# Performance work log

Hardware: AMD Instinct MI355X
Metric: run time of the kernel (lower is better)

The kernel has to match this reference:

```python
import jax, jax.numpy as jnp
import numpy as np

D_MODEL = 1024
N_HEADS = 16
D_K = D_MODEL // N_HEADS


def setup_inputs() -> dict:
    key = jax.random.key(0)
    k1, k2, k3 = jax.random.split(key, 3)
    x = jax.random.normal(k1, (4, 2048, D_MODEL), dtype=jnp.float32)
    # torch nn.Linear(d, 3d, bias=False): y = x @ W.T ; we store W.T directly as (in, out)
    w_qkv = jax.random.normal(k2, (D_MODEL, 3 * D_MODEL), dtype=jnp.float32) * (1.0 / np.sqrt(D_MODEL))
    w_out = jax.random.normal(k3, (D_MODEL, D_MODEL), dtype=jnp.float32) * (1.0 / np.sqrt(D_MODEL))
    return {"x": x, "w_qkv": w_qkv, "w_out": w_out}


def reference(x, w_qkv, w_out):
    B, T, D = x.shape
    qkv = jnp.einsum('btd,de->bte', x, w_qkv)  # (B,T,3D)
    q, k, v = jnp.split(qkv, 3, axis=-1)
    # split heads -> (B,H,T,d_k)
    def split_heads(t):
        return t.reshape(B, T, N_HEADS, D_K).transpose(0, 2, 1, 3)
    q, k, v = split_heads(q), split_heads(k), split_heads(v)
    scale = 1.0 / np.sqrt(D_K).astype(np.float32)
    scores = jnp.einsum('bhqd,bhkd->bhqk', q, k) * scale  # (B,H,T,T)
    causal = jnp.triu(jnp.full((T, T), -jnp.inf, dtype=scores.dtype), k=1)
    scores = scores + causal[None, None]
    weights = jax.nn.softmax(scores, axis=-1)
    attn = jnp.einsum('bhqk,bhkd->bhqd', weights, v)
    attn = attn.transpose(0, 2, 1, 3).reshape(B, T, D)
    return jnp.einsum('btd,de->bte', attn, w_out)
```

## Files before the change

kernel.cpp:

```cpp
#include <hip/hip_runtime.h>
#include <hip/hip_bf16.h>

typedef short short8 __attribute__((ext_vector_type(8)));
typedef float f32x4 __attribute__((ext_vector_type(4)));
typedef float f32x16 __attribute__((ext_vector_type(16)));

#define MFMA16(a, b, c) __builtin_amdgcn_mfma_f32_16x16x32_bf16((a), (b), (c), 0, 0, 0)
#define MFMA32(a, b, c) __builtin_amdgcn_mfma_f32_32x32x16_bf16((a), (b), (c), 0, 0, 0)

#define GLOAD16(gp, lp)                                                    \
    __builtin_amdgcn_global_load_lds(                                      \
        (const __attribute__((address_space(1))) unsigned int*)(gp),       \
        (__attribute__((address_space(3))) unsigned int*)(lp), 16, 0, 0)

__device__ __forceinline__ unsigned short f2b(float x) {
    unsigned int u = __float_as_uint(x);
    unsigned int r = u + 0x7FFFu + ((u >> 16) & 1u);
    return (unsigned short)(r >> 16);
}

#if __has_builtin(__builtin_amdgcn_cvt_pk_bf16_f32)
__device__ __forceinline__ unsigned pack2(float a, float b) {
    auto v = __builtin_amdgcn_cvt_pk_bf16_f32(a, b);
    unsigned u;
    __builtin_memcpy(&u, &v, 4);
    return u;
}
#else
__device__ __forceinline__ unsigned pack2(float a, float b) {
    return (unsigned)f2b(a) | ((unsigned)f2b(b) << 16);
}
#endif

__global__ __launch_bounds__(256) void cast4_kernel(const float* __restrict__ in,
                                                    unsigned short* __restrict__ out,
                                                    int n4) {
    int i = blockIdx.x * 256 + threadIdx.x;
    if (i < n4) {
        float4 v = ((const float4*)in)[i];
        ushort4 o;
        o.x = f2b(v.x); o.y = f2b(v.y); o.z = f2b(v.z); o.w = f2b(v.w);
        ((ushort4*)out)[i] = o;
    }
}

__global__ __launch_bounds__(256) void transpose_cast_f32(const float* __restrict__ in,
                                                          unsigned short* __restrict__ out,
                                                          int K, int N) {
    __shared__ unsigned short Ls[64 * 66];
    const int k0 = blockIdx.y * 64, n0 = blockIdx.x * 64;
    const int tid = threadIdx.x;
    const int krow = tid >> 4, nc4 = (tid & 15) * 4;
#pragma unroll
    for (int p = 0; p < 4; p++) {
        float4 v = *(const float4*)(in + (size_t)(k0 + krow + p * 16) * N + n0 + nc4);
        unsigned* d32 = (unsigned*)(Ls + (krow + p * 16) * 66 + nc4);
        d32[0] = pack2(v.x, v.y);
        d32[1] = pack2(v.z, v.w);
    }
    __syncthreads();
    const int n = tid >> 3, kc = (tid & 7) * 8;
#pragma unroll
    for (int p = 0; p < 2; p++) {
        int nn = n + p * 32;
        unsigned short w[8];
#pragma unroll
        for (int j = 0; j < 8; j++) w[j] = Ls[(kc + j) * 66 + nn];
        *(short8*)(out + (size_t)(n0 + nn) * K + k0 + kc) = *(short8*)w;
    }
}

__global__ __launch_bounds__(256) void gemm_qkv(const unsigned short* __restrict__ A,
                                                const unsigned short* __restrict__ Bt,
                                                unsigned short* __restrict__ Qb,
                                                unsigned short* __restrict__ Kb,
                                                unsigned short* __restrict__ Vt) {
    const int K = 1024, lda = 1024;
    __shared__ unsigned short As[128 * 64];
    __shared__ unsigned short Bs[128 * 64];

    const int tid  = threadIdx.x;
    const int wave = tid >> 6;
    const int lane = tid & 63;
    const int l32  = lane & 31;
    const int hi   = lane >> 5;
    const int m0 = blockIdx.y * 128;
    const int n0 = blockIdx.x * 128;
    const int wm = (wave >> 1) * 64;
    const int wn = (wave & 1) * 64;

    const int rl = lane >> 3;
    const int sc = ((lane & 7) ^ rl) * 8;

    const unsigned short* Ag[4]; unsigned short* Al[4];
    const unsigned short* Bg[4]; unsigned short* Bl[4];
#pragma unroll
    for (int cc = 0; cc < 4; cc++) {
        Ag[cc] = A  + (size_t)(m0 + wave * 32 + cc * 8 + rl) * lda + sc;
        Bg[cc] = Bt + (size_t)(n0 + wave * 32 + cc * 8 + rl) * K + sc;
        Al[cc] = As + (wave * 4 + cc) * 512;
        Bl[cc] = Bs + (wave * 4 + cc) * 512;
    }

    f32x16 acc[2][2] = {};

    for (int k0 = 0; k0 < K; k0 += 64) {
        __syncthreads();
#pragma unroll
        for (int cc = 0; cc < 4; cc++) GLOAD16(Ag[cc] + k0, Al[cc]);
#pragma unroll
        for (int cc = 0; cc < 4; cc++) GLOAD16(Bg[cc] + k0, Bl[cc]);
        __syncthreads();

#pragma unroll
        for (int ks = 0; ks < 4; ks++) {
            const int ch = (((ks * 2 + hi) ^ (l32 & 7))) * 8;
            short8 a0 = *(const short8*)(As + (wm + l32) * 64 + ch);
            short8 a1 = *(const short8*)(As + (wm + 32 + l32) * 64 + ch);
            short8 b0 = *(const short8*)(Bs + (wn + l32) * 64 + ch);
            short8 b1 = *(const short8*)(Bs + (wn + 32 + l32) * 64 + ch);
            acc[0][0] = MFMA32(a0, b0, acc[0][0]);
            acc[0][1] = MFMA32(a0, b1, acc[0][1]);
            acc[1][0] = MFMA32(a1, b0, acc[1][0]);
            acc[1][1] = MFMA32(a1, b1, acc[1][1]);
        }
    }

    if (n0 < 2048) {
        unsigned short* outp = (n0 < 1024) ? Qb : Kb;
        const int cb = (n0 < 1024) ? n0 : n0 - 1024;
        const float QS = (n0 < 1024) ? 0.125f * 1.44269504f : 1.0f;
#pragma unroll
        for (int i = 0; i < 2; i++)
#pragma unroll
            for (int j = 0; j < 2; j++)
#pragma unroll
                for (int r = 0; r < 16; r++) {
                    int row = m0 + wm + i * 32 + (r & 3) + 8 * (r >> 2) + 4 * hi;
                    int col = cb + wn + j * 32 + l32;
                    outp[(size_t)row * 1024 + col] = f2b(acc[i][j][r] * QS);
                }
    } else {
        const int b = m0 >> 11;
        const int t0b = m0 & 2047;
        const int hbase = (n0 - 2048) >> 6;
        unsigned short* smem = As;
        __syncthreads();
#pragma unroll
        for (int p = 0; p < 2; p++) {
            if ((wave & 1) == p) {
#pragma unroll
                for (int i = 0; i < 2; i++)
#pragma unroll
                    for (int j = 0; j < 2; j++) {
                        const int c = j * 32 + l32;
#pragma unroll
                        for (int rg = 0; rg < 4; rg++) {
                            const int rowbase = wm + i * 32 + rg * 8 + 4 * hi;
                            uint2 v;
                            v.x = pack2(acc[i][j][4 * rg + 0], acc[i][j][4 * rg + 1]);
                            v.y = pack2(acc[i][j][4 * rg + 2], acc[i][j][4 * rg + 3]);
                            const int w = c * 64 + ((rowbase >> 1) ^ (4 * (c & 7)));
                            *(uint2*)(smem + 2 * w) = v;
                        }
                    }
            }
            __syncthreads();
#pragma unroll
            for (int it = 0; it < 4; it++) {
                const int id = it * 256 + tid;
                const int c = id >> 4, rg = id & 15;
                const int w = c * 64 + ((rg * 4) ^ (4 * (c & 7)));
                short8 v = *(const short8*)(smem + 2 * w);
                const int h = hbase + p;
                *(short8*)(Vt + ((size_t)((b * 16 + h) * 64 + c)) * 2048 + t0b + rg * 8) = v;
            }
            __syncthreads();
        }
    }
}

__global__ __launch_bounds__(256) void gemm_out(const unsigned short* __restrict__ A,
                                                const unsigned short* __restrict__ Bt,
                                                float* __restrict__ C) {
    const int K = 1024, lda = 1024;
    __shared__ unsigned short As[64 * 64];
    __shared__ unsigned short Bs[128 * 64];

    const int tid  = threadIdx.x;
    const int wave = tid >> 6;
    const int lane = tid & 63;
    const int l32  = lane & 31;
    const int hi   = lane >> 5;
    const int m0 = blockIdx.y * 64;
    const int n0 = blockIdx.x * 128;
    const int wm = (wave >> 1) * 32;
    const int wn = (wave & 1) * 64;

    const int rl = lane >> 3;
    const int sc = ((lane & 7) ^ rl) * 8;

    const unsigned short* Ag[2]; unsigned short* Al[2];
#pragma unroll
    for (int cc = 0; cc < 2; cc++) {
        Ag[cc] = A + (size_t)(m0 + wave * 16 + cc * 8 + rl) * lda + sc;
        Al[cc] = As + (wave * 2 + cc) * 512;
    }
    const unsigned short* Bg[4]; unsigned short* Bl[4];
#pragma unroll
    for (int cc = 0; cc < 4; cc++) {
        Bg[cc] = Bt + (size_t)(n0 + wave * 32 + cc * 8 + rl) * K + sc;
        Bl[cc] = Bs + (wave * 4 + cc) * 512;
    }

    f32x16 acc[2] = {};

    for (int k0 = 0; k0 < K; k0 += 64) {
        __syncthreads();
#pragma unroll
        for (int cc = 0; cc < 2; cc++) GLOAD16(Ag[cc] + k0, Al[cc]);
#pragma unroll
        for (int cc = 0; cc < 4; cc++) GLOAD16(Bg[cc] + k0, Bl[cc]);
        __syncthreads();

#pragma unroll
        for (int ks = 0; ks < 4; ks++) {
            const int ch = (((ks * 2 + hi) ^ (l32 & 7))) * 8;
            short8 a  = *(const short8*)(As + (wm + l32) * 64 + ch);
            short8 b0 = *(const short8*)(Bs + (wn + l32) * 64 + ch);
            short8 b1 = *(const short8*)(Bs + (wn + 32 + l32) * 64 + ch);
            acc[0] = MFMA32(a, b0, acc[0]);
            acc[1] = MFMA32(a, b1, acc[1]);
        }
    }

#pragma unroll
    for (int j = 0; j < 2; j++)
#pragma unroll
        for (int r = 0; r < 16; r++) {
            int row = m0 + wm + (r & 3) + 8 * (r >> 2) + 4 * hi;
            int col = n0 + wn + j * 32 + l32;
            C[(size_t)row * 1024 + col] = acc[j][r];
        }
}

__global__ __launch_bounds__(256) void attention_kernel(const unsigned short* Qb,
                                                        const unsigned short* Kb,
                                                        const unsigned short* Vt,
                                                        unsigned short* attn) {
    const int T = 2048;
    const int bi = blockIdx.x;
    const int qb = 31 - (bi >> 6);
    const int hb = bi & 63;
    const int b = hb >> 4, h = hb & 15;
    const int qb0 = qb * 64;
    const int tid = threadIdx.x, wave = tid >> 6, lane = tid & 63;
    const int l16 = lane & 15, quad = lane >> 4;
    const int qw0 = qb0 + wave * 16;

    const unsigned short* Qp  = Qb + (size_t)b * T * 1024 + h * 64;
    const unsigned short* Kp  = Kb + (size_t)b * T * 1024 + h * 64;
    const unsigned short* Vbh = Vt + ((size_t)(b * 16 + h) * 64) * 2048;

    __shared__ unsigned short Ks[2][64 * 32];
    __shared__ unsigned short Vts[2][64 * 32];
    __shared__ unsigned short Ps[4][16 * 40];
    unsigned short* Psw = Ps[wave];

    short8 qf[2];
#pragma unroll
    for (int kd = 0; kd < 2; kd++)
        qf[kd] = *(const short8*)(Qp + (size_t)(qw0 + l16) * 1024 + kd * 32 + quad * 8);

    f32x4 o[4] = {};
    float l_acc = 0.f;

    const int srow = lane >> 2;
    const int scol = (((lane & 3) ^ ((lane >> 3) & 3)) * 8);
    const int sw8  = ((l16 >> 1) & 3) * 8;
    const size_t ktstep = (wave < 2) ? (size_t)64 * 1024 : (size_t)64;
    const size_t cstep  = (wave < 2) ? (size_t)16 * 1024 : (size_t)16 * T;
    const unsigned short* g0 = (wave < 2)
            ? Kp + (size_t)srow * 1024 + wave * 32 + scol
            : Vbh + (size_t)srow * T + (wave - 2) * 32 + scol;
    unsigned short* l0 = (wave < 2) ? Ks[wave] : Vts[wave - 2];

    for (int kt = 0; kt <= qb; kt++) {
        const int tk0 = kt * 64;
        const unsigned short* g = g0 + (size_t)kt * ktstep;
        __syncthreads();
#pragma unroll
        for (int c = 0; c < 4; c++) GLOAD16(g + c * cstep, l0 + c * 512);
        __syncthreads();

#pragma unroll
        for (int th = 0; th < 2; th++) {
            if (tk0 + th * 32 > qw0 + 15) continue;

            f32x4 s[2];
            bool act[2];
#pragma unroll
            for (int mi = 0; mi < 2; mi++) {
                const int t0 = tk0 + (th * 2 + mi) * 16;
                act[mi] = (t0 <= qw0 + 15);
                s[mi] = (f32x4){0.f, 0.f, 0.f, 0.f};
                if (act[mi]) {
                    const int row = (th * 2 + mi) * 16 + l16;
                    short8 kf0 = *(const short8*)(Ks[0] + row * 32 + (quad * 8 ^ sw8));
                    short8 kf1 = *(const short8*)(Ks[1] + row * 32 + (quad * 8 ^ sw8));
                    s[mi] = MFMA16(kf0, qf[0], s[mi]);
                    s[mi] = MFMA16(kf1, qf[1], s[mi]);
                }
            }
#pragma unroll
            for (int mi = 0; mi < 2; mi++) {
                const int t0 = tk0 + (th * 2 + mi) * 16;
                unsigned pk0 = 0, pk1 = 0;
                if (act[mi]) {
                    const bool full = (t0 + 15) <= qw0;
                    float p[4];
#pragma unroll
                    for (int r = 0; r < 4; r++) {
                        float e = __builtin_amdgcn_exp2f(s[mi][r]);
                        if (!full)
                            e = (t0 + quad * 4 + r <= qw0 + l16) ? e : 0.f;
                        p[r] = e;
                    }
                    l_acc += (p[0] + p[1]) + (p[2] + p[3]);
                    pk0 = pack2(p[0], p[1]);
                    pk1 = pack2(p[2], p[3]);
                }
                uint2 pr; pr.x = pk0; pr.y = pk1;
                *(uint2*)(Psw + l16 * 40 + mi * 16 + quad * 4) = pr;
            }
            short8 pf = *(const short8*)(Psw + l16 * 40 + quad * 8);
#pragma unroll
            for (int dt = 0; dt < 4; dt++) {
                short8 vf = *(const short8*)(Vts[th] + (dt * 16 + l16) * 32 + (quad * 8 ^ sw8));
                o[dt] = MFMA16(vf, pf, o[dt]);
            }
        }
    }

    float l = l_acc;
    l += __shfl_xor(l, 16);
    l += __shfl_xor(l, 32);
    const float rl2 = 1.f / l;
    const int q = qw0 + l16;
#pragma unroll
    for (int dt = 0; dt < 4; dt++) {
        ushort4 wv;
        wv.x = f2b(o[dt][0] * rl2);
        wv.y = f2b(o[dt][1] * rl2);
        wv.z = f2b(o[dt][2] * rl2);
        wv.w = f2b(o[dt][3] * rl2);
        *(ushort4*)(attn + (size_t)(b * T + q) * 1024 + h * 64 + dt * 16 + quad * 4) = wv;
    }
}

extern "C" void kernel_launch(void* const* d_in, const int* in_sizes, int n_in,
                              void* d_out, int out_size, void* d_ws, size_t ws_size,
                              hipStream_t stream) {
    const float* x     = (const float*)d_in[0];
    const float* w_qkv = (const float*)d_in[1];
    const float* w_out = (const float*)d_in[2];
    float* out = (float*)d_out;

    const int M = 8192, D = 1024, E = 3072;
    const size_t MB = 1048576;

    char* ws = (char*)d_ws;
    unsigned short* xb    = (unsigned short*)ws;
    unsigned short* wqkvT = (unsigned short*)(ws + 16 * MB);
    unsigned short* woutT = (unsigned short*)(ws + 22 * MB);
    unsigned short* Qb    = (unsigned short*)(ws + 24 * MB);
    unsigned short* Kb    = (unsigned short*)(ws + 40 * MB);
    unsigned short* Vt    = (unsigned short*)(ws + 56 * MB);

    cast4_kernel<<<M * D / 4 / 256, 256, 0, stream>>>(x, xb, M * D / 4);
    transpose_cast_f32<<<dim3(E / 64, D / 64), 256, 0, stream>>>(w_qkv, wqkvT, D, E);
    transpose_cast_f32<<<dim3(D / 64, D / 64), 256, 0, stream>>>(w_out, woutT, D, D);

    gemm_qkv<<<dim3(E / 128, M / 128), 256, 0, stream>>>(xb, wqkvT, Qb, Kb, Vt);

    attention_kernel<<<dim3(2048), 256, 0, stream>>>(Qb, Kb, Vt, Qb);

    gemm_out<<<dim3(D / 128, M / 64), 256, 0, stream>>>(Qb, woutT, out);
}
```

Measured before the change: 269.5 us.

## Double-buffer LDS tiles in GEMM and attention kernels to overlap loads

Converts the QKV GEMM, the output GEMM and the attention K/V loop from load-then-compute with two barriers per step to a double-buffered scheme. The next tile's global_load_lds is issued into the alternate buffer right after a single barrier, while the current buffer is consumed by MFMAs. This is meant to hide global-memory latency and remove one barrier per iteration. In exchange, shared memory per block roughly doubles, which may lower the number of resident blocks per CU.

```diff
diff --git a/kernel.cpp b/kernel.cpp
--- a/kernel.cpp
+++ b/kernel.cpp
@@ -76,8 +76,8 @@
                                                 unsigned short* __restrict__ Kb,
                                                 unsigned short* __restrict__ Vt) {
     const int K = 1024, lda = 1024;
-    __shared__ unsigned short As[128 * 64];
-    __shared__ unsigned short Bs[128 * 64];
+    __shared__ unsigned short As[2 * 8192];
+    __shared__ unsigned short Bs[2 * 8192];
 
     const int tid  = threadIdx.x;
     const int wave = tid >> 6;
@@ -104,21 +104,29 @@
 
     f32x16 acc[2][2] = {};
 
-    for (int k0 = 0; k0 < K; k0 += 64) {
+#pragma unroll
+    for (int cc = 0; cc < 4; cc++) GLOAD16(Ag[cc], Al[cc]);
+#pragma unroll
+    for (int cc = 0; cc < 4; cc++) GLOAD16(Bg[cc], Bl[cc]);
+
+    int buf = 0;
+    for (int k0 = 0; k0 < K; k0 += 64, buf ^= 1) {
         __syncthreads();
-#pragma unroll
-        for (int cc = 0; cc < 4; cc++) GLOAD16(Ag[cc] + k0, Al[cc]);
-#pragma unroll
-        for (int cc = 0; cc < 4; cc++) GLOAD16(Bg[cc] + k0, Bl[cc]);
-        __syncthreads();
-
+        if (k0 + 64 < K) {
+#pragma unroll
+            for (int cc = 0; cc < 4; cc++) GLOAD16(Ag[cc] + k0 + 64, Al[cc] + (buf ^ 1) * 8192);
+#pragma unroll
+            for (int cc = 0; cc < 4; cc++) GLOAD16(Bg[cc] + k0 + 64, Bl[cc] + (buf ^ 1) * 8192);
+        }
+        const unsigned short* Asb = As + buf * 8192;
+        const unsigned short* Bsb = Bs + buf * 8192;
 #pragma unroll
         for (int ks = 0; ks < 4; ks++) {
             const int ch = (((ks * 2 + hi) ^ (l32 & 7))) * 8;
-            short8 a0 = *(const short8*)(As + (wm + l32) * 64 + ch);
-            short8 a1 = *(const short8*)(As + (wm + 32 + l32) * 64 + ch);
-            short8 b0 = *(const short8*)(Bs + (wn + l32) * 64 + ch);
-            short8 b1 = *(const short8*)(Bs + (wn + 32 + l32) * 64 + ch);
+            short8 a0 = *(const short8*)(Asb + (wm + l32) * 64 + ch);
+            short8 a1 = *(const short8*)(Asb + (wm + 32 + l32) * 64 + ch);
+            short8 b0 = *(const short8*)(Bsb + (wn + l32) * 64 + ch);
+            short8 b1 = *(const short8*)(Bsb + (wn + 32 + l32) * 64 + ch);
             acc[0][0] = MFMA32(a0, b0, acc[0][0]);
             acc[0][1] = MFMA32(a0, b1, acc[0][1]);
             acc[1][0] = MFMA32(a1, b0, acc[1][0]);
@@ -184,8 +192,8 @@
                                                 const unsigned short* __restrict__ Bt,
                                                 float* __restrict__ C) {
     const int K = 1024, lda = 1024;
-    __shared__ unsigned short As[64 * 64];
-    __shared__ unsigned short Bs[128 * 64];
+    __shared__ unsigned short As[2 * 4096];
+    __shared__ unsigned short Bs[2 * 8192];
 
     const int tid  = threadIdx.x;
     const int wave = tid >> 6;
@@ -215,20 +223,28 @@
 
     f32x16 acc[2] = {};
 
-    for (int k0 = 0; k0 < K; k0 += 64) {
+#pragma unroll
+    for (int cc = 0; cc < 2; cc++) GLOAD16(Ag[cc], Al[cc]);
+#pragma unroll
+    for (int cc = 0; cc < 4; cc++) GLOAD16(Bg[cc], Bl[cc]);
+
+    int buf = 0;
+    for (int k0 = 0; k0 < K; k0 += 64, buf ^= 1) {
         __syncthreads();
-#pragma unroll
-        for (int cc = 0; cc < 2; cc++) GLOAD16(Ag[cc] + k0, Al[cc]);
-#pragma unroll
-        for (int cc = 0; cc < 4; cc++) GLOAD16(Bg[cc] + k0, Bl[cc]);
-        __syncthreads();
-
+        if (k0 + 64 < K) {
+#pragma unroll
+            for (int cc = 0; cc < 2; cc++) GLOAD16(Ag[cc] + k0 + 64, Al[cc] + (buf ^ 1) * 4096);
+#pragma unroll
+            for (int cc = 0; cc < 4; cc++) GLOAD16(Bg[cc] + k0 + 64, Bl[cc] + (buf ^ 1) * 8192);
+        }
+        const unsigned short* Asb = As + buf * 4096;
+        const unsigned short* Bsb = Bs + buf * 8192;
 #pragma unroll
         for (int ks = 0; ks < 4; ks++) {
             const int ch = (((ks * 2 + hi) ^ (l32 & 7))) * 8;
-            short8 a  = *(const short8*)(As + (wm + l32) * 64 + ch);
-            short8 b0 = *(const short8*)(Bs + (wn + l32) * 64 + ch);
-            short8 b1 = *(const short8*)(Bs + (wn + 32 + l32) * 64 + ch);
+            short8 a  = *(const short8*)(Asb + (wm + l32) * 64 + ch);
+            short8 b0 = *(const short8*)(Bsb + (wn + l32) * 64 + ch);
+            short8 b1 = *(const short8*)(Bsb + (wn + 32 + l32) * 64 + ch);
             acc[0] = MFMA32(a, b0, acc[0]);
             acc[1] = MFMA32(a, b1, acc[1]);
         }
@@ -262,8 +278,7 @@
     const unsigned short* Kp  = Kb + (size_t)b * T * 1024 + h * 64;
     const unsigned short* Vbh = Vt + ((size_t)(b * 16 + h) * 64) * 2048;
 
-    __shared__ unsigned short Ks[2][64 * 32];
-    __shared__ unsigned short Vts[2][64 * 32];
+    __shared__ unsigned short KVs[2][4][64 * 32];
     __shared__ unsigned short Ps[4][16 * 40];
     unsigned short* Psw = Ps[wave];
 
@@ -283,15 +298,21 @@
     const unsigned short* g0 = (wave < 2)
             ? Kp + (size_t)srow * 1024 + wave * 32 + scol
             : Vbh + (size_t)srow * T + (wave - 2) * 32 + scol;
-    unsigned short* l0 = (wave < 2) ? Ks[wave] : Vts[wave - 2];
+
+#pragma unroll
+    for (int c = 0; c < 4; c++) GLOAD16(g0 + c * cstep, KVs[0][wave] + c * 512);
 
     for (int kt = 0; kt <= qb; kt++) {
+        const int buf = kt & 1;
         const int tk0 = kt * 64;
-        const unsigned short* g = g0 + (size_t)kt * ktstep;
         __syncthreads();
-#pragma unroll
-        for (int c = 0; c < 4; c++) GLOAD16(g + c * cstep, l0 + c * 512);
-        __syncthreads();
+        if (kt < qb) {
+            const unsigned short* g = g0 + (size_t)(kt + 1) * ktstep;
+#pragma unroll
+            for (int c = 0; c < 4; c++) GLOAD16(g + c * cstep, KVs[buf ^ 1][wave] + c * 512);
+        }
+        const unsigned short* Ks0 = KVs[buf][0];
+        const unsigned short* Ks1 = KVs[buf][1];
 
 #pragma unroll
         for (int th = 0; th < 2; th++) {
@@ -306,8 +327,8 @@
                 s[mi] = (f32x4){0.f, 0.f, 0.f, 0.f};
                 if (act[mi]) {
                     const int row = (th * 2 + mi) * 16 + l16;
-                    short8 kf0 = *(const short8*)(Ks[0] + row * 32 + (quad * 8 ^ sw8));
-                    short8 kf1 = *(const short8*)(Ks[1] + row * 32 + (quad * 8 ^ sw8));
+                    short8 kf0 = *(const short8*)(Ks0 + row * 32 + (quad * 8 ^ sw8));
+                    short8 kf1 = *(const short8*)(Ks1 + row * 32 + (quad * 8 ^ sw8));
                     s[mi] = MFMA16(kf0, qf[0], s[mi]);
                     s[mi] = MFMA16(kf1, qf[1], s[mi]);
                 }
@@ -336,7 +357,7 @@
             short8 pf = *(const short8*)(Psw + l16 * 40 + quad * 8);
 #pragma unroll
             for (int dt = 0; dt < 4; dt++) {
-                short8 vf = *(const short8*)(Vts[th] + (dt * 16 + l16) * 32 + (quad * 8 ^ sw8));
+                short8 vf = *(const short8*)(KVs[buf][2 + th] + (dt * 16 + l16) * 32 + (quad * 8 ^ sw8));
                 o[dt] = MFMA16(vf, pf, o[dt]);
             }
         }
```

After: 283.1 us. 5.0% more time.
